# Kernel optimization log

Hardware: AMD Instinct MI355X
Metric: run time of the kernel (lower is better)

Reference implementation:

```python
import jax, jax.numpy as jnp
import numpy as np

N, E, IN_DIM, HID, L = 50000, 800000, 64, 64, 3
EDGE_DIM = 2 * HID + 2  # src_h | dst_h | edge_feat


def setup_inputs() -> dict:
    key = jax.random.key(0)
    ks = jax.random.split(key, 32)
    s = 0.05
    inp = {
        "h": jax.random.normal(ks[0], (N, IN_DIM), jnp.float32),
        "e": jax.random.normal(ks[1], (E, 2), jnp.float32),
        "src": jax.random.randint(ks[2], (E,), 0, N),
        "dst": jax.random.randint(ks[3], (E,), 0, N),
        # input embedding
        "emb_W": jax.random.normal(ks[4], (IN_DIM, HID), jnp.float32) * s,
        "emb_b": jnp.zeros((HID,), jnp.float32),
        # per-GIN-layer params (stacked over L)
        "eps": jnp.zeros((L,), jnp.float32),  # learn_eps init 0
        "mlp_W1": jax.random.normal(ks[5], (L, HID, HID), jnp.float32) * s,
        "mlp_b1": jnp.zeros((L, HID), jnp.float32),
        "mlp_bn_s": jnp.ones((L, HID), jnp.float32),   # eval-mode BN folded: x*s+sh
        "mlp_bn_sh": jnp.zeros((L, HID), jnp.float32),
        "mlp_W2": jax.random.normal(ks[6], (L, HID, HID), jnp.float32) * s,
        "mlp_b2": jnp.zeros((L, HID), jnp.float32),
        "apply_bn_s": jnp.ones((L, HID), jnp.float32),
        "apply_bn_sh": jnp.zeros((L, HID), jnp.float32),
        "gin_bn_s": jnp.ones((L, HID), jnp.float32),
        "gin_bn_sh": jnp.zeros((L, HID), jnp.float32),
        # prediction heads (L+1 of them)
        "pred_W1": jax.random.normal(ks[7], (L + 1, EDGE_DIM, HID), jnp.float32) * s,
        "pred_b1": jnp.zeros((L + 1, HID), jnp.float32),
        "pred_W2": jax.random.normal(ks[8], (L + 1, HID, 1), jnp.float32) * s,
        "pred_b2": jnp.zeros((L + 1, 1), jnp.float32),
    }
    return inp


def reference(h, e, src, dst, emb_W, emb_b, eps,
              mlp_W1, mlp_b1, mlp_bn_s, mlp_bn_sh, mlp_W2, mlp_b2,
              apply_bn_s, apply_bn_sh, gin_bn_s, gin_bn_sh,
              pred_W1, pred_b1, pred_W2, pred_b2):
    n = h.shape[0]
    bn = lambda x, sc, sh: x * sc + sh  # eval-mode batchnorm (folded scale/shift)

    h = h @ emb_W + emb_b  # [N, HID]

    def edge_feat(hh):
        # gather node features onto edges: [E, 2*HID+2]
        return jnp.concatenate([hh[src], hh[dst], e], axis=1)

    def pred(ef, i):
        z = jax.nn.relu(ef @ pred_W1[i] + pred_b1[i])
        return z @ pred_W2[i] + pred_b2[i]  # [E, 1]

    score = pred(edge_feat(h), 0)
    for i in range(L):
        h_in = h
        # GIN sum aggregation: copy src features, sum at dst
        neigh = jax.ops.segment_sum(h[src], dst, num_segments=n)
        x = (1.0 + eps[i]) * h + neigh
        # MLP: Linear -> BN -> ReLU -> Linear
        x = jax.nn.relu(bn(x @ mlp_W1[i] + mlp_b1[i], mlp_bn_s[i], mlp_bn_sh[i]))
        x = x @ mlp_W2[i] + mlp_b2[i]
        # ApplyNodeFunc: BN -> ReLU
        x = jax.nn.relu(bn(x, apply_bn_s[i], apply_bn_sh[i]))
        # GINLayer post: BN -> ReLU -> residual (dropout=0 in eval)
        x = jax.nn.relu(bn(x, gin_bn_s[i], gin_bn_sh[i]))
        h = h_in + x
        score = score + pred(edge_feat(h), i + 1)
    return jax.nn.relu(score)
```

## Files before the change

kernel.cpp:

```cpp
#include <hip/hip_runtime.h>

typedef unsigned short ushort_t;
typedef unsigned int uint_t;

static __device__ __forceinline__ ushort_t f2bf(float f) {
    uint_t u = __float_as_uint(f);
    uint_t r = (u + 0x7FFFu + ((u >> 16) & 1u)) >> 16;
    return (ushort_t)r;
}
static __device__ __forceinline__ float bf2f(ushort_t u) {
    return __uint_as_float(((uint_t)u) << 16);
}
static __device__ __forceinline__ float bf2f_lo(uint_t u) {
    return __uint_as_float(u << 16);
}
static __device__ __forceinline__ float bf2f_hi(uint_t u) {
    return __uint_as_float(u & 0xffff0000u);
}
static __device__ __forceinline__ uint_t pack2(float lo, float hi) {
    return (uint_t)f2bf(lo) | ((uint_t)f2bf(hi) << 16);
}

static __device__ __forceinline__ float edge_p2(
    uint_t ax, uint_t ay, float4 brow, float ex, float ey,
    float4 wc0, float4 wc1, float4 w2v)
{
    float z0 = bf2f_lo(ax) + brow.x + ex*wc0.x + ey*wc1.x; z0 = fmaxf(z0, 0.f);
    float z1 = bf2f_hi(ax) + brow.y + ex*wc0.y + ey*wc1.y; z1 = fmaxf(z1, 0.f);
    float z2 = bf2f_lo(ay) + brow.z + ex*wc0.z + ey*wc1.z; z2 = fmaxf(z2, 0.f);
    float z3 = bf2f_hi(ay) + brow.w + ex*wc0.w + ey*wc1.w; z3 = fmaxf(z3, 0.f);
    return z0*w2v.x + z1*w2v.y + z2*w2v.z + z3*w2v.w;
}

#define RED16(p) { p += __shfl_xor(p,1); p += __shfl_xor(p,2); \
                   p += __shfl_xor(p,4); p += __shfl_xor(p,8); }

__global__ __launch_bounds__(256) void k_count(
    const int* __restrict__ dst, int* __restrict__ deg, int E)
{
    int e = blockIdx.x * 256 + threadIdx.x;
    if (e < E) atomicAdd(&deg[dst[e]], 1);
}

static __device__ __forceinline__ int deg_bucket(int d) {
    return d >= 63 ? 0 : (63 - d);
}

__global__ __launch_bounds__(1024) void k_scanA(
    const int* __restrict__ deg, int* __restrict__ partial,
    int* __restrict__ bsum, int* __restrict__ bcnt, int N)
{
    __shared__ int wsum[16];
    __shared__ int hist[64];
    int tid = threadIdx.x, lane = tid & 63, wid = tid >> 6;
    if (tid < 64) hist[tid] = 0;
    __syncthreads();
    int idx = blockIdx.x * 1024 + tid;
    int v = (idx < N) ? deg[idx] : 0;
    if (idx < N) atomicAdd(&hist[deg_bucket(v)], 1);
    int x = v;
#pragma unroll
    for (int o = 1; o < 64; o <<= 1) {
        int t = __shfl_up(x, o, 64);
        if (lane >= o) x += t;
    }
    if (lane == 63) wsum[wid] = x;
    __syncthreads();
    if (wid == 0) {
        int s = (lane < 16) ? wsum[lane] : 0;
#pragma unroll
        for (int o = 1; o < 16; o <<= 1) {
            int t = __shfl_up(s, o, 64);
            if (lane >= o) s += t;
        }
        if (lane < 16) wsum[lane] = s;
    }
    __syncthreads();
    int woff = (wid > 0) ? wsum[wid - 1] : 0;
    if (idx < N) partial[idx] = woff + x - v;
    if (tid == 0) bsum[blockIdx.x] = wsum[15];
    __syncthreads();
    if (tid < 64 && hist[tid]) atomicAdd(&bcnt[tid], hist[tid]);
}

__global__ __launch_bounds__(256) void k_scanB(
    int* __restrict__ bsum, int nb, int* __restrict__ totalp)
{
    __shared__ int s[256];
    int tid = threadIdx.x;
    int v = (tid < nb) ? bsum[tid] : 0;
    s[tid] = v;
    __syncthreads();
#pragma unroll
    for (int off = 1; off < 256; off <<= 1) {
        int t = (tid >= off) ? s[tid - off] : 0;
        __syncthreads();
        s[tid] += t;
        __syncthreads();
    }
    if (tid < nb) bsum[tid] = s[tid] - v;
    if (tid == 0) totalp[0] = s[255];
}

__global__ __launch_bounds__(256) void k_scanC(
    int* __restrict__ offsets, const int* __restrict__ bsum,
    int* __restrict__ cursor, int N)
{
    int idx = blockIdx.x * 256 + threadIdx.x;
    if (idx >= N) return;
    int o = offsets[idx] + bsum[idx >> 10];
    offsets[idx] = o;
    cursor[idx] = o;
}

__global__ __launch_bounds__(256) void k_fill(
    const int* __restrict__ src, const int* __restrict__ dst,
    const float* __restrict__ ep, int* __restrict__ cursor,
    int4* __restrict__ entries, int E)
{
    int ei = blockIdx.x * 256 + threadIdx.x;
    if (ei >= E) return;
    int pos = atomicAdd(&cursor[dst[ei]], 1);
    float2 ev = *(const float2*)(ep + 2 * (size_t)ei);
    entries[pos] = make_int4(src[ei], ei, __float_as_int(ev.x), __float_as_int(ev.y));
}

__global__ __launch_bounds__(64) void k_bscan(
    int* __restrict__ bcnt, int* __restrict__ bcur)
{
    int lane = threadIdx.x;
    int v = bcnt[lane];
    int x = v;
#pragma unroll
    for (int o = 1; o < 64; o <<= 1) {
        int t = __shfl_up(x, o, 64);
        if (lane >= o) x += t;
    }
    bcur[lane] = x - v;
}

__global__ __launch_bounds__(256) void k_bfill(
    const int* __restrict__ offsets, int* __restrict__ bcur,
    int* __restrict__ perm, int N)
{
    __shared__ int hist[64];
    __shared__ int lbase[64];
    int tid = threadIdx.x;
    if (tid < 64) hist[tid] = 0;
    __syncthreads();
    int idx = blockIdx.x * 256 + tid;
    int b = 0, rank = 0;
    bool valid = (idx < N);
    if (valid) {
        int d = offsets[idx + 1] - offsets[idx];
        b = deg_bucket(d);
        rank = atomicAdd(&hist[b], 1);
    }
    __syncthreads();
    if (tid < 64) lbase[tid] = hist[tid] ? atomicAdd(&bcur[tid], hist[tid]) : 0;
    __syncthreads();
    if (valid) perm[lbase[b] + rank] = idx;
}

template <int WRITE>
static __device__ __forceinline__ void epi_tables16(
    float (*xs)[68], int row, int li, int r, float4 o,
    const float* __restrict__ WAn, const float* __restrict__ bAn,
    const float* __restrict__ WBn,
    ushort_t* __restrict__ tab_out, ushort_t* __restrict__ B_out)
{
    xs[row][4*li+0] = o.x; xs[row][4*li+1] = o.y;
    xs[row][4*li+2] = o.z; xs[row][4*li+3] = o.w;
    float4 aA = *(const float4*)(bAn + 4 * li);
    float4 aB = make_float4(0.f, 0.f, 0.f, 0.f);
#pragma unroll
    for (int k = 0; k < 64; k++) {
        float xk = xs[row][k];
        float4 wa = *(const float4*)(WAn + k * 64 + 4 * li);
        float4 wb = *(const float4*)(WBn + k * 64 + 4 * li);
        aA.x += xk * wa.x; aA.y += xk * wa.y; aA.z += xk * wa.z; aA.w += xk * wa.w;
        aB.x += xk * wb.x; aB.y += xk * wb.y; aB.z += xk * wb.z; aB.w += xk * wb.w;
    }
    if (WRITE == 1) {
        int4 cw;
        cw.x = (int)pack2(aA.x, aA.y);
        cw.y = (int)pack2(aA.z, aA.w);
        cw.z = (int)pack2(o.x, o.y);
        cw.w = (int)pack2(o.z, o.w);
        *(int4*)(tab_out + (size_t)r * 128 + li * 8) = cw;
    } else {
        ushort4 oa;
        oa.x = f2bf(aA.x); oa.y = f2bf(aA.y); oa.z = f2bf(aA.z); oa.w = f2bf(aA.w);
        *(ushort4*)(tab_out + (size_t)r * 64 + 4 * li) = oa;
    }
    ushort4 ob;
    ob.x = f2bf(aB.x); ob.y = f2bf(aB.y); ob.z = f2bf(aB.z); ob.w = f2bf(aB.w);
    *(ushort4*)(B_out + (size_t)r * 64 + 4 * li) = ob;
}

__global__ __launch_bounds__(256) void k_embed_ab(
    const float* __restrict__ in, const float* __restrict__ W,
    const float* __restrict__ bias, float* __restrict__ hout,
    const float* __restrict__ WA, const float* __restrict__ bA,
    const float* __restrict__ WB,
    ushort_t* __restrict__ comb_out, ushort_t* __restrict__ B_out, int N)
{
    __shared__ float xs[16][68];
    const int row16 = threadIdx.x >> 4;
    const int li    = threadIdx.x & 15;
    const int r     = blockIdx.x * 16 + row16;
    if (r >= N) return;
    float4 x4 = *(const float4*)(in + (size_t)r * 64 + 4 * li);
    xs[row16][4*li+0] = x4.x; xs[row16][4*li+1] = x4.y;
    xs[row16][4*li+2] = x4.z; xs[row16][4*li+3] = x4.w;
    float4 acc = *(const float4*)(bias + 4 * li);
#pragma unroll
    for (int k = 0; k < 64; k++) {
        float xk = xs[row16][k];
        float4 wv = *(const float4*)(W + k * 64 + 4 * li);
        acc.x += xk * wv.x; acc.y += xk * wv.y;
        acc.z += xk * wv.z; acc.w += xk * wv.w;
    }
    *(float4*)(hout + (size_t)r * 64 + 4 * li) = acc;
    epi_tables16<1>(xs, row16, li, r, acc, WA, bA, WB, comb_out, B_out);
}

__global__ __launch_bounds__(256) void k_tables(
    const float* __restrict__ h,
    const float* __restrict__ WA, const float* __restrict__ bA,
    const float* __restrict__ WB,
    ushort_t* __restrict__ comb_out, ushort_t* __restrict__ B_out, int N)
{
    __shared__ float xs[16][68];
    const int row16 = threadIdx.x >> 4;
    const int li    = threadIdx.x & 15;
    const int r     = blockIdx.x * 16 + row16;
    if (r >= N) return;
    float4 o = *(const float4*)(h + (size_t)r * 64 + 4 * li);
    epi_tables16<1>(xs, row16, li, r, o, WA, bA, WB, comb_out, B_out);
}

template <int MODE, int EPI>
__global__ __launch_bounds__(256) void k_fused(
    const float* __restrict__ h, float* __restrict__ hout,
    const ushort_t* __restrict__ comb, const ushort_t* __restrict__ Bm,
    const int4* __restrict__ entries, const int* __restrict__ offsets,
    const int* __restrict__ perm,
    float* __restrict__ score_csr,
    const float* __restrict__ Wc, const float* __restrict__ W2v,
    const float* __restrict__ b2p, const float* __restrict__ epsp,
    const float* __restrict__ W1, const float* __restrict__ b1,
    const float* __restrict__ s1, const float* __restrict__ sh1,
    const float* __restrict__ W2, const float* __restrict__ b2,
    const float* __restrict__ as_, const float* __restrict__ ash,
    const float* __restrict__ gs, const float* __restrict__ gsh,
    const float* __restrict__ WAn, const float* __restrict__ bAn,
    const float* __restrict__ WBn,
    ushort_t* __restrict__ tab_out, ushort_t* __restrict__ B_out, int N)
{
    __shared__ float xs[16][68];
    const int row16 = threadIdx.x >> 4;
    const int li    = threadIdx.x & 15;
    const int idx   = blockIdx.x * 16 + row16;
    if (idx >= N) return;
    const int r = perm[idx];

    const float4 wc0 = *(const float4*)(Wc + li*4);
    const float4 wc1 = *(const float4*)(Wc + 64 + li*4);
    const float4 w2v = *(const float4*)(W2v + li*4);
    const float bb2 = b2p[0];
    ushort4 bu = *(const ushort4*)(Bm + (size_t)r * 64 + li*4);
    const float4 brow = make_float4(bf2f(bu.x), bf2f(bu.y), bf2f(bu.z), bf2f(bu.w));

    const int beg = offsets[r], end = offsets[r + 1];
    float4 acc = make_float4(0.f, 0.f, 0.f, 0.f);

    int k = beg;
    for (; k + 3 < end; k += 4) {
        int4 e0 = entries[k], e1 = entries[k+1], e2 = entries[k+2], e3 = entries[k+3];
        int4 c0 = *(const int4*)(comb + (size_t)e0.x * 128 + li * 8);
        int4 c1 = *(const int4*)(comb + (size_t)e1.x * 128 + li * 8);
        int4 c2 = *(const int4*)(comb + (size_t)e2.x * 128 + li * 8);
        int4 c3 = *(const int4*)(comb + (size_t)e3.x * 128 + li * 8);
        acc.x += bf2f_lo(c0.z) + bf2f_lo(c1.z) + bf2f_lo(c2.z) + bf2f_lo(c3.z);
        acc.y += bf2f_hi(c0.z) + bf2f_hi(c1.z) + bf2f_hi(c2.z) + bf2f_hi(c3.z);
        acc.z += bf2f_lo(c0.w) + bf2f_lo(c1.w) + bf2f_lo(c2.w) + bf2f_lo(c3.w);
        acc.w += bf2f_hi(c0.w) + bf2f_hi(c1.w) + bf2f_hi(c2.w) + bf2f_hi(c3.w);
        float p0 = edge_p2((uint_t)c0.x, (uint_t)c0.y, brow,
                           __int_as_float(e0.z), __int_as_float(e0.w), wc0, wc1, w2v);
        float p1 = edge_p2((uint_t)c1.x, (uint_t)c1.y, brow,
                           __int_as_float(e1.z), __int_as_float(e1.w), wc0, wc1, w2v);
        float p2 = edge_p2((uint_t)c2.x, (uint_t)c2.y, brow,
                           __int_as_float(e2.z), __int_as_float(e2.w), wc0, wc1, w2v);
        float p3 = edge_p2((uint_t)c3.x, (uint_t)c3.y, brow,
                           __int_as_float(e3.z), __int_as_float(e3.w), wc0, wc1, w2v);
        RED16(p0) RED16(p1) RED16(p2) RED16(p3)
        if (li == 0) {
            if (MODE == 0) {
                score_csr[k]   = p0 + bb2; score_csr[k+1] = p1 + bb2;
                score_csr[k+2] = p2 + bb2; score_csr[k+3] = p3 + bb2;
            } else {
                score_csr[k]   += p0 + bb2; score_csr[k+1] += p1 + bb2;
                score_csr[k+2] += p2 + bb2; score_csr[k+3] += p3 + bb2;
            }
        }
    }
    for (; k < end; k++) {
        int4 e0 = entries[k];
        int4 c0 = *(const int4*)(comb + (size_t)e0.x * 128 + li * 8);
        acc.x += bf2f_lo((uint_t)c0.z); acc.y += bf2f_hi((uint_t)c0.z);
        acc.z += bf2f_lo((uint_t)c0.w); acc.w += bf2f_hi((uint_t)c0.w);
        float p0 = edge_p2((uint_t)c0.x, (uint_t)c0.y, brow,
                           __int_as_float(e0.z), __int_as_float(e0.w), wc0, wc1, w2v);
        RED16(p0)
        if (li == 0) {
            if (MODE == 0) score_csr[k] = p0 + bb2;
            else           score_csr[k] += p0 + bb2;
        }
    }

    const float epsv = 1.0f + epsp[0];
    float4 hv = *(const float4*)(h + (size_t)r * 64 + 4 * li);
    xs[row16][4*li+0] = epsv * hv.x + acc.x;
    xs[row16][4*li+1] = epsv * hv.y + acc.y;
    xs[row16][4*li+2] = epsv * hv.z + acc.z;
    xs[row16][4*li+3] = epsv * hv.w + acc.w;

    float4 t = *(const float4*)(b1 + 4 * li);
#pragma unroll
    for (int kk = 0; kk < 64; kk++) {
        float xk = xs[row16][kk];
        float4 wv = *(const float4*)(W1 + kk * 64 + 4 * li);
        t.x += xk * wv.x; t.y += xk * wv.y; t.z += xk * wv.z; t.w += xk * wv.w;
    }
    {
        float4 sc = *(const float4*)(s1 + 4 * li);
        float4 sh = *(const float4*)(sh1 + 4 * li);
        t.x = fmaxf(t.x * sc.x + sh.x, 0.f);
        t.y = fmaxf(t.y * sc.y + sh.y, 0.f);
        t.z = fmaxf(t.z * sc.z + sh.z, 0.f);
        t.w = fmaxf(t.w * sc.w + sh.w, 0.f);
    }
    xs[row16][4*li+0] = t.x; xs[row16][4*li+1] = t.y;
    xs[row16][4*li+2] = t.z; xs[row16][4*li+3] = t.w;

    float4 u = *(const float4*)(b2 + 4 * li);
#pragma unroll
    for (int kk = 0; kk < 64; kk++) {
        float tk = xs[row16][kk];
        float4 wv = *(const float4*)(W2 + kk * 64 + 4 * li);
        u.x += tk * wv.x; u.y += tk * wv.y; u.z += tk * wv.z; u.w += tk * wv.w;
    }
    {
        float4 sc = *(const float4*)(as_ + 4 * li);
        float4 sh = *(const float4*)(ash + 4 * li);
        u.x = fmaxf(u.x * sc.x + sh.x, 0.f);
        u.y = fmaxf(u.y * sc.y + sh.y, 0.f);
        u.z = fmaxf(u.z * sc.z + sh.z, 0.f);
        u.w = fmaxf(u.w * sc.w + sh.w, 0.f);
        sc = *(const float4*)(gs + 4 * li);
        sh = *(const float4*)(gsh + 4 * li);
        u.x = fmaxf(u.x * sc.x + sh.x, 0.f);
        u.y = fmaxf(u.y * sc.y + sh.y, 0.f);
        u.z = fmaxf(u.z * sc.z + sh.z, 0.f);
        u.w = fmaxf(u.w * sc.w + sh.w, 0.f);
    }
    float4 o = make_float4(hv.x + u.x, hv.y + u.y, hv.z + u.z, hv.w + u.w);
    *(float4*)(hout + (size_t)r * 64 + 4 * li) = o;

    if (EPI == 1)
        epi_tables16<1>(xs, row16, li, r, o, WAn, bAn, WBn, tab_out, B_out);
    else if (EPI == 2)
        epi_tables16<2>(xs, row16, li, r, o, WAn, bAn, WBn, tab_out, B_out);
}

template <int COMPACT>
__global__ __launch_bounds__(256) void k_head(
    const ushort_t* __restrict__ Atab,
    const ushort_t* __restrict__ Bm,
    const int4* __restrict__ entries, const int* __restrict__ offsets,
    const int* __restrict__ perm,
    const float* __restrict__ score_csr, float* __restrict__ score_out,
    const float* __restrict__ Wc, const float* __restrict__ W2v,
    const float* __restrict__ b2p, int N)
{
    const int row16 = threadIdx.x >> 4;
    const int li    = threadIdx.x & 15;
    const int idx   = blockIdx.x * 16 + row16;
    if (idx >= N) return;
    const int r = perm[idx];

    const float4 wc0 = *(const float4*)(Wc + li*4);
    const float4 wc1 = *(const float4*)(Wc + 64 + li*4);
    const float4 w2v = *(const float4*)(W2v + li*4);
    const float bb2 = b2p[0];
    ushort4 bu = *(const ushort4*)(Bm + (size_t)r * 64 + li*4);
    const float4 brow = make_float4(bf2f(bu.x), bf2f(bu.y), bf2f(bu.z), bf2f(bu.w));

    const int beg = offsets[r], end = offsets[r + 1];

#define ALOAD(s, ax, ay) { \
    if (COMPACT) { \
        ushort4 a_ = *(const ushort4*)(Atab + (size_t)(s) * 64 + li * 4); \
        ax = (uint_t)a_.x | ((uint_t)a_.y << 16); \
        ay = (uint_t)a_.z | ((uint_t)a_.w << 16); \
    } else { \
        int2 d_ = *(const int2*)(Atab + (size_t)(s) * 128 + li * 8); \
        ax = (uint_t)d_.x; ay = (uint_t)d_.y; \
    } }
#define HSCOR(kk, e_, ax, ay) { \
    float p_ = edge_p2(ax, ay, brow, __int_as_float((e_).z), __int_as_float((e_).w), \
                       wc0, wc1, w2v); \
    RED16(p_) \
    if (li == 0) score_out[(e_).y] = fmaxf(score_csr[kk] + p_ + bb2, 0.f); }

    int k = beg;
    for (; k + 3 < end; k += 4) {
        int4 e0 = entries[k], e1 = entries[k+1], e2 = entries[k+2], e3 = entries[k+3];
        uint_t ax0, ay0, ax1, ay1, ax2, ay2, ax3, ay3;
        ALOAD(e0.x, ax0, ay0) ALOAD(e1.x, ax1, ay1)
        ALOAD(e2.x, ax2, ay2) ALOAD(e3.x, ax3, ay3)
        HSCOR(k, e0, ax0, ay0) HSCOR(k+1, e1, ax1, ay1)
        HSCOR(k+2, e2, ax2, ay2) HSCOR(k+3, e3, ax3, ay3)
    }
    for (; k < end; k++) {
        int4 e0 = entries[k];
        uint_t ax0, ay0;
        ALOAD(e0.x, ax0, ay0)
        HSCOR(k, e0, ax0, ay0)
    }
#undef ALOAD
#undef HSCOR
}

extern "C" void kernel_launch(void* const* d_in, const int* in_sizes, int n_in,
                              void* d_out, int out_size, void* d_ws, size_t ws_size,
                              hipStream_t stream) {
    const float* h_in  = (const float*)d_in[0];
    const float* e     = (const float*)d_in[1];
    const int*   src   = (const int*)d_in[2];
    const int*   dst   = (const int*)d_in[3];
    const float* emb_W = (const float*)d_in[4];
    const float* emb_b = (const float*)d_in[5];
    const float* eps   = (const float*)d_in[6];
    const float* mW1   = (const float*)d_in[7];
    const float* mb1   = (const float*)d_in[8];
    const float* mbs   = (const float*)d_in[9];
    const float* mbsh  = (const float*)d_in[10];
    const float* mW2   = (const float*)d_in[11];
    const float* mb2   = (const float*)d_in[12];
    const float* as_   = (const float*)d_in[13];
    const float* ash   = (const float*)d_in[14];
    const float* gs    = (const float*)d_in[15];
    const float* gsh   = (const float*)d_in[16];
    const float* pW1   = (const float*)d_in[17];
    const float* pb1   = (const float*)d_in[18];
    const float* pW2   = (const float*)d_in[19];
    const float* pb2   = (const float*)d_in[20];

    const int N  = in_sizes[0] / 64;
    const int E  = in_sizes[2];
    const int Lr = in_sizes[6];
    const size_t nrow = (size_t)N * 64;

    float* score = (float*)d_out;

    char* wp = (char*)d_ws;
    auto take = [&](size_t b) -> char* {
        char* p = wp; wp += (b + 255) & ~(size_t)255; return p;
    };
    float*    h0        = (float*)take(nrow * 4);
    float*    h1        = (float*)take(nrow * 4);
    ushort_t* comb0     = (ushort_t*)take(nrow * 4);
    ushort_t* B0        = (ushort_t*)take(nrow * 2);
    int4*     entries   = (int4*)take((size_t)E * 16);
    float*    score_csr = (float*)take((size_t)E * 4);
    int*      offsets   = (int*)take((size_t)(N + 1) * 4);
    int*      cursor    = (int*)take((size_t)N * 4);
    int*      bsum      = (int*)take(1024);
    int*      perm      = (int*)take((size_t)N * 4);
    int*      bcnt      = (int*)take(64 * 4);
    int*      bcur      = (int*)take(64 * 4);
    ushort_t* comb1     = (ushort_t*)take(nrow * 4);
    ushort_t* B1        = (ushort_t*)take(nrow * 2);
    ushort_t* Afin      = (ushort_t*)take(nrow * 2);
    size_t need_epi = (size_t)(wp - (char*)d_ws);

    const bool use_epi = ws_size >= need_epi;

    const int rowBlocks = (N + 15) / 16;
    const int edgeGrid  = (E + 255) / 256;
    const int nb        = (N + 1023) / 1024;

    hipMemsetAsync(cursor, 0, (size_t)N * sizeof(int), stream);
    hipMemsetAsync(bcnt, 0, 64 * sizeof(int), stream);
    k_count<<<edgeGrid, 256, 0, stream>>>(dst, cursor, E);
    k_scanA<<<nb, 1024, 0, stream>>>(cursor, offsets, bsum, bcnt, N);
    k_scanB<<<1, 256, 0, stream>>>(bsum, nb, offsets + N);
    k_scanC<<<(N + 255) / 256, 256, 0, stream>>>(offsets, bsum, cursor, N);
    k_fill<<<edgeGrid, 256, 0, stream>>>(src, dst, e, cursor, entries, E);

    k_bscan<<<1, 64, 0, stream>>>(bcnt, bcur);
    k_bfill<<<(N + 255) / 256, 256, 0, stream>>>(offsets, bcur, perm, N);

    k_embed_ab<<<rowBlocks, 256, 0, stream>>>(
        h_in, emb_W, emb_b, h0, pW1, pb1, pW1 + 64 * 64, comb0, B0, N);

    float* hcur = h0;       float* hnext = h1;
    ushort_t* Ccur = comb0; ushort_t* Cnxt = use_epi ? comb1 : comb0;
    ushort_t* Bcur = B0;    ushort_t* Bnxt = use_epi ? B1 : B0;

    for (int i = 0; i < Lr; i++) {
        const float* pw  = pW1 + (size_t)i * 130 * 64;
        const float* Wc  = pw + 128 * 64;
        const float* w2  = pW2 + (size_t)i * 64;
        const float* b2  = pb2 + i;
        const float* pwn = pW1 + (size_t)(i + 1) * 130 * 64;
        const float* gW1 = mW1 + (size_t)i * 64 * 64;
        const float* gW2 = mW2 + (size_t)i * 64 * 64;
        const bool last = (i == Lr - 1);

        if (use_epi) {
            ushort_t* tout = last ? Afin : Cnxt;
            if (i == 0 && !last)
                k_fused<0,1><<<rowBlocks, 256, 0, stream>>>(
                    hcur, hnext, Ccur, Bcur, entries, offsets, perm, score_csr,
                    Wc, w2, b2, eps + i,
                    gW1, mb1 + i*64, mbs + i*64, mbsh + i*64, gW2, mb2 + i*64,
                    as_ + i*64, ash + i*64, gs + i*64, gsh + i*64,
                    pwn, pb1 + (i+1)*64, pwn + 64*64, tout, Bnxt, N);
            else if (i == 0 && last)
                k_fused<0,2><<<rowBlocks, 256, 0, stream>>>(
                    hcur, hnext, Ccur, Bcur, entries, offsets, perm, score_csr,
                    Wc, w2, b2, eps + i,
                    gW1, mb1 + i*64, mbs + i*64, mbsh + i*64, gW2, mb2 + i*64,
                    as_ + i*64, ash + i*64, gs + i*64, gsh + i*64,
                    pwn, pb1 + (i+1)*64, pwn + 64*64, tout, Bnxt, N);
            else if (!last)
                k_fused<1,1><<<rowBlocks, 256, 0, stream>>>(
                    hcur, hnext, Ccur, Bcur, entries, offsets, perm, score_csr,
                    Wc, w2, b2, eps + i,
                    gW1, mb1 + i*64, mbs + i*64, mbsh + i*64, gW2, mb2 + i*64,
                    as_ + i*64, ash + i*64, gs + i*64, gsh + i*64,
                    pwn, pb1 + (i+1)*64, pwn + 64*64, tout, Bnxt, N);
            else
                k_fused<1,2><<<rowBlocks, 256, 0, stream>>>(
                    hcur, hnext, Ccur, Bcur, entries, offsets, perm, score_csr,
                    Wc, w2, b2, eps + i,
                    gW1, mb1 + i*64, mbs + i*64, mbsh + i*64, gW2, mb2 + i*64,
                    as_ + i*64, ash + i*64, gs + i*64, gsh + i*64,
                    pwn, pb1 + (i+1)*64, pwn + 64*64, tout, Bnxt, N);
            { ushort_t* t = Ccur; Ccur = Cnxt; Cnxt = t; }
            { ushort_t* t = Bcur; Bcur = Bnxt; Bnxt = t; }
        } else {
            if (i == 0)
                k_fused<0,0><<<rowBlocks, 256, 0, stream>>>(
                    hcur, hnext, Ccur, Bcur, entries, offsets, perm, score_csr,
                    Wc, w2, b2, eps + i,
                    gW1, mb1 + i*64, mbs + i*64, mbsh + i*64, gW2, mb2 + i*64,
                    as_ + i*64, ash + i*64, gs + i*64, gsh + i*64,
                    nullptr, nullptr, nullptr, nullptr, nullptr, N);
            else
                k_fused<1,0><<<rowBlocks, 256, 0, stream>>>(
                    hcur, hnext, Ccur, Bcur, entries, offsets, perm, score_csr,
                    Wc, w2, b2, eps + i,
                    gW1, mb1 + i*64, mbs + i*64, mbsh + i*64, gW2, mb2 + i*64,
                    as_ + i*64, ash + i*64, gs + i*64, gsh + i*64,
                    nullptr, nullptr, nullptr, nullptr, nullptr, N);
            k_tables<<<rowBlocks, 256, 0, stream>>>(
                hnext, pwn, pb1 + (i+1)*64, pwn + 64*64, Ccur, Bcur, N);
        }
        { float* t = hcur; hcur = hnext; hnext = t; }
    }

    {
        const float* pw = pW1 + (size_t)Lr * 130 * 64;
        const float* Wc = pw + 128 * 64;
        const float* w2 = pW2 + (size_t)Lr * 64;
        const float* b2 = pb2 + Lr;
        if (use_epi)
            k_head<1><<<rowBlocks, 256, 0, stream>>>(
                Afin, Bcur, entries, offsets, perm, score_csr, score,
                Wc, w2, b2, N);
        else
            k_head<0><<<rowBlocks, 256, 0, stream>>>(
                Ccur, Bcur, entries, offsets, perm, score_csr, score,
                Wc, w2, b2, N);
    }
}
```

Baseline: 587.8 us.

## Compact edge entries to 8 bytes and mux-reduce four edge scores

Adds a conversion pass that packs each CSR entry into an int2 holding the source index and the two edge features as bf16. The fused layer kernels read this compact form, halving entry traffic per edge. Both the layer and head kernels now use a butterfly mux-reduction that combines four edge partial sums with fewer shuffles and writes them from four lanes at once. Storing edge features in bf16 costs precision, and the extra conversion kernel and workspace are only used when the workspace is large enough.

```diff
diff --git a/kernel.cpp b/kernel.cpp
--- a/kernel.cpp
+++ b/kernel.cpp
@@ -35,6 +35,19 @@
 #define RED16(p) { p += __shfl_xor(p,1); p += __shfl_xor(p,2); \
                    p += __shfl_xor(p,4); p += __shfl_xor(p,8); }
 
+#define MUXRED4(p0,p1,p2,p3,li,r) { \
+    float m1a_ = ((li)&1) ? (p1) : (p0); \
+    float n1a_ = ((li)&1) ? (p0) : (p1); \
+    float m1b_ = ((li)&1) ? (p3) : (p2); \
+    float n1b_ = ((li)&1) ? (p2) : (p3); \
+    float ra_ = m1a_ + __shfl_xor(n1a_, 1); \
+    float rb_ = m1b_ + __shfl_xor(n1b_, 1); \
+    float m2_ = ((li)&2) ? rb_ : ra_; \
+    float n2_ = ((li)&2) ? ra_ : rb_; \
+    r = m2_ + __shfl_xor(n2_, 2); \
+    r += __shfl_xor(r, 4); \
+    r += __shfl_xor(r, 8); }
+
 __global__ __launch_bounds__(256) void k_count(
     const int* __restrict__ dst, int* __restrict__ deg, int E)
 {
@@ -123,6 +136,16 @@
     int pos = atomicAdd(&cursor[dst[ei]], 1);
     float2 ev = *(const float2*)(ep + 2 * (size_t)ei);
     entries[pos] = make_int4(src[ei], ei, __float_as_int(ev.x), __float_as_int(ev.y));
+}
+
+__global__ __launch_bounds__(256) void k_convert(
+    const int4* __restrict__ entries, int2* __restrict__ entries8, int E)
+{
+    int k = blockIdx.x * 256 + threadIdx.x;
+    if (k >= E) return;
+    int4 v = entries[k];
+    entries8[k] = make_int2(v.x,
+        (int)pack2(__int_as_float(v.z), __int_as_float(v.w)));
 }
 
 __global__ __launch_bounds__(64) void k_bscan(
@@ -240,12 +263,12 @@
     epi_tables16<1>(xs, row16, li, r, o, WA, bA, WB, comb_out, B_out);
 }
 
-template <int MODE, int EPI>
+template <int MODE, int EPI, int E8>
 __global__ __launch_bounds__(256) void k_fused(
     const float* __restrict__ h, float* __restrict__ hout,
     const ushort_t* __restrict__ comb, const ushort_t* __restrict__ Bm,
-    const int4* __restrict__ entries, const int* __restrict__ offsets,
-    const int* __restrict__ perm,
+    const int4* __restrict__ entries, const int2* __restrict__ entries8,
+    const int* __restrict__ offsets, const int* __restrict__ perm,
     float* __restrict__ score_csr,
     const float* __restrict__ Wc, const float* __restrict__ W2v,
     const float* __restrict__ b2p, const float* __restrict__ epsp,
@@ -277,41 +300,59 @@
 
     int k = beg;
     for (; k + 3 < end; k += 4) {
-        int4 e0 = entries[k], e1 = entries[k+1], e2 = entries[k+2], e3 = entries[k+3];
-        int4 c0 = *(const int4*)(comb + (size_t)e0.x * 128 + li * 8);
-        int4 c1 = *(const int4*)(comb + (size_t)e1.x * 128 + li * 8);
-        int4 c2 = *(const int4*)(comb + (size_t)e2.x * 128 + li * 8);
-        int4 c3 = *(const int4*)(comb + (size_t)e3.x * 128 + li * 8);
-        acc.x += bf2f_lo(c0.z) + bf2f_lo(c1.z) + bf2f_lo(c2.z) + bf2f_lo(c3.z);
-        acc.y += bf2f_hi(c0.z) + bf2f_hi(c1.z) + bf2f_hi(c2.z) + bf2f_hi(c3.z);
-        acc.z += bf2f_lo(c0.w) + bf2f_lo(c1.w) + bf2f_lo(c2.w) + bf2f_lo(c3.w);
-        acc.w += bf2f_hi(c0.w) + bf2f_hi(c1.w) + bf2f_hi(c2.w) + bf2f_hi(c3.w);
-        float p0 = edge_p2((uint_t)c0.x, (uint_t)c0.y, brow,
-                           __int_as_float(e0.z), __int_as_float(e0.w), wc0, wc1, w2v);
-        float p1 = edge_p2((uint_t)c1.x, (uint_t)c1.y, brow,
-                           __int_as_float(e1.z), __int_as_float(e1.w), wc0, wc1, w2v);
-        float p2 = edge_p2((uint_t)c2.x, (uint_t)c2.y, brow,
-                           __int_as_float(e2.z), __int_as_float(e2.w), wc0, wc1, w2v);
-        float p3 = edge_p2((uint_t)c3.x, (uint_t)c3.y, brow,
-                           __int_as_float(e3.z), __int_as_float(e3.w), wc0, wc1, w2v);
-        RED16(p0) RED16(p1) RED16(p2) RED16(p3)
-        if (li == 0) {
-            if (MODE == 0) {
-                score_csr[k]   = p0 + bb2; score_csr[k+1] = p1 + bb2;
-                score_csr[k+2] = p2 + bb2; score_csr[k+3] = p3 + bb2;
-            } else {
-                score_csr[k]   += p0 + bb2; score_csr[k+1] += p1 + bb2;
-                score_csr[k+2] += p2 + bb2; score_csr[k+3] += p3 + bb2;
-            }
+        int s0, s1e, s2e, s3e;
+        float x0, y0, x1, y1, x2, y2, x3, y3;
+        if (E8) {
+            int2 q0 = entries8[k],   q1 = entries8[k+1];
+            int2 q2 = entries8[k+2], q3 = entries8[k+3];
+            s0 = q0.x; x0 = bf2f_lo((uint_t)q0.y); y0 = bf2f_hi((uint_t)q0.y);
+            s1e = q1.x; x1 = bf2f_lo((uint_t)q1.y); y1 = bf2f_hi((uint_t)q1.y);
+            s2e = q2.x; x2 = bf2f_lo((uint_t)q2.y); y2 = bf2f_hi((uint_t)q2.y);
+            s3e = q3.x; x3 = bf2f_lo((uint_t)q3.y); y3 = bf2f_hi((uint_t)q3.y);
+        } else {
+            int4 q0 = entries[k],   q1 = entries[k+1];
+            int4 q2 = entries[k+2], q3 = entries[k+3];
+            s0 = q0.x; x0 = __int_as_float(q0.z); y0 = __int_as_float(q0.w);
+            s1e = q1.x; x1 = __int_as_float(q1.z); y1 = __int_as_float(q1.w);
+            s2e = q2.x; x2 = __int_as_float(q2.z); y2 = __int_as_float(q2.w);
+            s3e = q3.x; x3 = __int_as_float(q3.z); y3 = __int_as_float(q3.w);
         }
+        int4 c0 = *(const int4*)(comb + (size_t)s0  * 128 + li * 8);
+        int4 c1 = *(const int4*)(comb + (size_t)s1e * 128 + li * 8);
+        int4 c2 = *(const int4*)(comb + (size_t)s2e * 128 + li * 8);
+        int4 c3 = *(const int4*)(comb + (size_t)s3e * 128 + li * 8);
+        acc.x += bf2f_lo((uint_t)c0.z) + bf2f_lo((uint_t)c1.z)
+               + bf2f_lo((uint_t)c2.z) + bf2f_lo((uint_t)c3.z);
+        acc.y += bf2f_hi((uint_t)c0.z) + bf2f_hi((uint_t)c1.z)
+               + bf2f_hi((uint_t)c2.z) + bf2f_hi((uint_t)c3.z);
+        acc.z += bf2f_lo((uint_t)c0.w) + bf2f_lo((uint_t)c1.w)
+               + bf2f_lo((uint_t)c2.w) + bf2f_lo((uint_t)c3.w);
+        acc.w += bf2f_hi((uint_t)c0.w) + bf2f_hi((uint_t)c1.w)
+               + bf2f_hi((uint_t)c2.w) + bf2f_hi((uint_t)c3.w);
+        float p0 = edge_p2((uint_t)c0.x, (uint_t)c0.y, brow, x0, y0, wc0, wc1, w2v);
+        float p1 = edge_p2((uint_t)c1.x, (uint_t)c1.y, brow, x1, y1, wc0, wc1, w2v);
+        float p2 = edge_p2((uint_t)c2.x, (uint_t)c2.y, brow, x2, y2, wc0, wc1, w2v);
+        float p3 = edge_p2((uint_t)c3.x, (uint_t)c3.y, brow, x3, y3, wc0, wc1, w2v);
+        float pr;
+        MUXRED4(p0, p1, p2, p3, li, pr)
+        if (li < 4) {
+            if (MODE == 0) score_csr[k + li] = pr + bb2;
+            else           score_csr[k + li] += pr + bb2;
+        }
     }
     for (; k < end; k++) {
-        int4 e0 = entries[k];
-        int4 c0 = *(const int4*)(comb + (size_t)e0.x * 128 + li * 8);
+        int s0; float x0, y0;
+        if (E8) {
+            int2 q0 = entries8[k];
+            s0 = q0.x; x0 = bf2f_lo((uint_t)q0.y); y0 = bf2f_hi((uint_t)q0.y);
+        } else {
+            int4 q0 = entries[k];
+            s0 = q0.x; x0 = __int_as_float(q0.z); y0 = __int_as_float(q0.w);
+        }
+        int4 c0 = *(const int4*)(comb + (size_t)s0 * 128 + li * 8);
         acc.x += bf2f_lo((uint_t)c0.z); acc.y += bf2f_hi((uint_t)c0.z);
         acc.z += bf2f_lo((uint_t)c0.w); acc.w += bf2f_hi((uint_t)c0.w);
-        float p0 = edge_p2((uint_t)c0.x, (uint_t)c0.y, brow,
-                           __int_as_float(e0.z), __int_as_float(e0.w), wc0, wc1, w2v);
+        float p0 = edge_p2((uint_t)c0.x, (uint_t)c0.y, brow, x0, y0, wc0, wc1, w2v);
         RED16(p0)
         if (li == 0) {
             if (MODE == 0) score_csr[k] = p0 + bb2;
@@ -408,11 +449,6 @@
         int2 d_ = *(const int2*)(Atab + (size_t)(s) * 128 + li * 8); \
         ax = (uint_t)d_.x; ay = (uint_t)d_.y; \
     } }
-#define HSCOR(kk, e_, ax, ay) { \
-    float p_ = edge_p2(ax, ay, brow, __int_as_float((e_).z), __int_as_float((e_).w), \
-                       wc0, wc1, w2v); \
-    RED16(p_) \
-    if (li == 0) score_out[(e_).y] = fmaxf(score_csr[kk] + p_ + bb2, 0.f); }
 
     int k = beg;
     for (; k + 3 < end; k += 4) {
@@ -420,17 +456,26 @@
         uint_t ax0, ay0, ax1, ay1, ax2, ay2, ax3, ay3;
         ALOAD(e0.x, ax0, ay0) ALOAD(e1.x, ax1, ay1)
         ALOAD(e2.x, ax2, ay2) ALOAD(e3.x, ax3, ay3)
-        HSCOR(k, e0, ax0, ay0) HSCOR(k+1, e1, ax1, ay1)
-        HSCOR(k+2, e2, ax2, ay2) HSCOR(k+3, e3, ax3, ay3)
+        float p0 = edge_p2(ax0, ay0, brow, __int_as_float(e0.z), __int_as_float(e0.w), wc0, wc1, w2v);
+        float p1 = edge_p2(ax1, ay1, brow, __int_as_float(e1.z), __int_as_float(e1.w), wc0, wc1, w2v);
+        float p2 = edge_p2(ax2, ay2, brow, __int_as_float(e2.z), __int_as_float(e2.w), wc0, wc1, w2v);
+        float p3 = edge_p2(ax3, ay3, brow, __int_as_float(e3.z), __int_as_float(e3.w), wc0, wc1, w2v);
+        float pr;
+        MUXRED4(p0, p1, p2, p3, li, pr)
+        if (li < 4) {
+            int eid = (li == 0) ? e0.y : (li == 1) ? e1.y : (li == 2) ? e2.y : e3.y;
+            score_out[eid] = fmaxf(score_csr[k + li] + pr + bb2, 0.f);
+        }
     }
     for (; k < end; k++) {
         int4 e0 = entries[k];
         uint_t ax0, ay0;
         ALOAD(e0.x, ax0, ay0)
-        HSCOR(k, e0, ax0, ay0)
+        float p0 = edge_p2(ax0, ay0, brow, __int_as_float(e0.z), __int_as_float(e0.w), wc0, wc1, w2v);
+        RED16(p0)
+        if (li == 0) score_out[e0.y] = fmaxf(score_csr[k] + p0 + bb2, 0.f);
     }
 #undef ALOAD
-#undef HSCOR
 }
 
 extern "C" void kernel_launch(void* const* d_in, const int* in_sizes, int n_in,
@@ -485,8 +530,11 @@
     ushort_t* B1        = (ushort_t*)take(nrow * 2);
     ushort_t* Afin      = (ushort_t*)take(nrow * 2);
     size_t need_epi = (size_t)(wp - (char*)d_ws);
+    int2*     entries8  = (int2*)take((size_t)E * 8);
+    size_t need_e8 = (size_t)(wp - (char*)d_ws);
 
     const bool use_epi = ws_size >= need_epi;
+    const bool use_e8  = ws_size >= need_e8;
 
     const int rowBlocks = (N + 15) / 16;
     const int edgeGrid  = (E + 255) / 256;
@@ -499,6 +547,8 @@
     k_scanB<<<1, 256, 0, stream>>>(bsum, nb, offsets + N);
     k_scanC<<<(N + 255) / 256, 256, 0, stream>>>(offsets, bsum, cursor, N);
     k_fill<<<edgeGrid, 256, 0, stream>>>(src, dst, e, cursor, entries, E);
+    if (use_e8)
+        k_convert<<<edgeGrid, 256, 0, stream>>>(entries, entries8, E);
 
     k_bscan<<<1, 64, 0, stream>>>(bcnt, bcur);
     k_bfill<<<(N + 255) / 256, 256, 0, stream>>>(offsets, bcur, perm, N);
@@ -509,6 +559,12 @@
     float* hcur = h0;       float* hnext = h1;
     ushort_t* Ccur = comb0; ushort_t* Cnxt = use_epi ? comb1 : comb0;
     ushort_t* Bcur = B0;    ushort_t* Bnxt = use_epi ? B1 : B0;
+
+#define LF(M, EP, E8s) k_fused<M, EP, E8s><<<rowBlocks, 256, 0, stream>>>( \
+    hcur, hnext, Ccur, Bcur, entries, entries8, offsets, perm, score_csr, \
+    Wc, w2, b2, eps + i, gW1, mb1 + i*64, mbs + i*64, mbsh + i*64, gW2, \
+    mb2 + i*64, as_ + i*64, ash + i*64, gs + i*64, gsh + i*64, \
+    pwn, pb1 + (i+1)*64, pwn + 64*64, tout, bout, N)
 
     for (int i = 0; i < Lr; i++) {
         const float* pw  = pW1 + (size_t)i * 130 * 64;
@@ -522,56 +578,31 @@
 
         if (use_epi) {
             ushort_t* tout = last ? Afin : Cnxt;
-            if (i == 0 && !last)
-                k_fused<0,1><<<rowBlocks, 256, 0, stream>>>(
-                    hcur, hnext, Ccur, Bcur, entries, offsets, perm, score_csr,
-                    Wc, w2, b2, eps + i,
-                    gW1, mb1 + i*64, mbs + i*64, mbsh + i*64, gW2, mb2 + i*64,
-                    as_ + i*64, ash + i*64, gs + i*64, gsh + i*64,
-                    pwn, pb1 + (i+1)*64, pwn + 64*64, tout, Bnxt, N);
-            else if (i == 0 && last)
-                k_fused<0,2><<<rowBlocks, 256, 0, stream>>>(
-                    hcur, hnext, Ccur, Bcur, entries, offsets, perm, score_csr,
-                    Wc, w2, b2, eps + i,
-                    gW1, mb1 + i*64, mbs + i*64, mbsh + i*64, gW2, mb2 + i*64,
-                    as_ + i*64, ash + i*64, gs + i*64, gsh + i*64,
-                    pwn, pb1 + (i+1)*64, pwn + 64*64, tout, Bnxt, N);
-            else if (!last)
-                k_fused<1,1><<<rowBlocks, 256, 0, stream>>>(
-                    hcur, hnext, Ccur, Bcur, entries, offsets, perm, score_csr,
-                    Wc, w2, b2, eps + i,
-                    gW1, mb1 + i*64, mbs + i*64, mbsh + i*64, gW2, mb2 + i*64,
-                    as_ + i*64, ash + i*64, gs + i*64, gsh + i*64,
-                    pwn, pb1 + (i+1)*64, pwn + 64*64, tout, Bnxt, N);
-            else
-                k_fused<1,2><<<rowBlocks, 256, 0, stream>>>(
-                    hcur, hnext, Ccur, Bcur, entries, offsets, perm, score_csr,
-                    Wc, w2, b2, eps + i,
-                    gW1, mb1 + i*64, mbs + i*64, mbsh + i*64, gW2, mb2 + i*64,
-                    as_ + i*64, ash + i*64, gs + i*64, gsh + i*64,
-                    pwn, pb1 + (i+1)*64, pwn + 64*64, tout, Bnxt, N);
+            ushort_t* bout = Bnxt;
+            if (use_e8) {
+                if (i == 0 && !last)      LF(0, 1, 1);
+                else if (i == 0 && last)  LF(0, 2, 1);
+                else if (!last)           LF(1, 1, 1);
+                else                      LF(1, 2, 1);
+            } else {
+                if (i == 0 && !last)      LF(0, 1, 0);
+                else if (i == 0 && last)  LF(0, 2, 0);
+                else if (!last)           LF(1, 1, 0);
+                else                      LF(1, 2, 0);
+            }
             { ushort_t* t = Ccur; Ccur = Cnxt; Cnxt = t; }
             { ushort_t* t = Bcur; Bcur = Bnxt; Bnxt = t; }
         } else {
-            if (i == 0)
-                k_fused<0,0><<<rowBlocks, 256, 0, stream>>>(
-                    hcur, hnext, Ccur, Bcur, entries, offsets, perm, score_csr,
-                    Wc, w2, b2, eps + i,
-                    gW1, mb1 + i*64, mbs + i*64, mbsh + i*64, gW2, mb2 + i*64,
-                    as_ + i*64, ash + i*64, gs + i*64, gsh + i*64,
-                    nullptr, nullptr, nullptr, nullptr, nullptr, N);
-            else
-                k_fused<1,0><<<rowBlocks, 256, 0, stream>>>(
-                    hcur, hnext, Ccur, Bcur, entries, offsets, perm, score_csr,
-                    Wc, w2, b2, eps + i,
-                    gW1, mb1 + i*64, mbs + i*64, mbsh + i*64, gW2, mb2 + i*64,
-                    as_ + i*64, ash + i*64, gs + i*64, gsh + i*64,
-                    nullptr, nullptr, nullptr, nullptr, nullptr, N);
+            ushort_t* tout = nullptr;
+            ushort_t* bout = nullptr;
+            if (i == 0) LF(0, 0, 0);
+            else        LF(1, 0, 0);
             k_tables<<<rowBlocks, 256, 0, stream>>>(
                 hnext, pwn, pb1 + (i+1)*64, pwn + 64*64, Ccur, Bcur, N);
         }
         { float* t = hcur; hcur = hnext; hnext = t; }
     }
+#undef LF
 
     {
         const float* pw = pW1 + (size_t)Lr * 130 * 64;
```

New measurement: 588.2 us. Within noise of the previous version (+0.1%).
